# Kernel tuning notes

Measured on AMD Instinct MI355X. Metric: run time of the kernel, lower is better.

The kernel has to match this reference:

```python
import jax, jax.numpy as jnp
import numpy as np
import math

B, T, C, H = 2, 2048, 1024, 16
HD = C // H
WINDOW = 256  # local_attn_ctx with attnblocksize=1


def setup_inputs() -> dict:
    key = jax.random.key(0)
    k1, k2, k3 = jax.random.split(key, 3)
    x = jax.random.normal(k1, (B, T, C), dtype=jnp.float32)
    Wqkv = jax.random.normal(k2, (C, 3 * C), dtype=jnp.float32) * 0.02
    bqkv = jnp.zeros((3 * C,), dtype=jnp.float32)
    Wproj = jax.random.normal(k3, (C, C), dtype=jnp.float32) * 0.02
    bproj = jnp.zeros((C,), dtype=jnp.float32)
    # 'local' block-sparse layout at token granularity: causal + sliding window
    i = np.arange(T)[:, None]
    j = np.arange(T)[None, :]
    mask = ((j <= i) & (i - j <= WINDOW)).astype(np.int32)
    return {"x": x, "Wqkv": Wqkv, "bqkv": bqkv, "Wproj": Wproj, "bproj": bproj,
            "mask": jnp.asarray(mask)}


def reference(x, Wqkv, bqkv, Wproj, bproj, mask):
    Bb, Tt, Cc = x.shape
    qkv = (x @ Wqkv + bqkv).reshape(Bb, Tt, 3, H, HD)  # [B,T,3,H,hd]
    q = jnp.transpose(qkv[:, :, 0], (0, 2, 1, 3))  # [B,H,T,hd]
    k = jnp.transpose(qkv[:, :, 1], (0, 2, 1, 3))
    v = jnp.transpose(qkv[:, :, 2], (0, 2, 1, 3))
    scale = 1.0 / math.sqrt(HD)
    att = jnp.einsum('bhqd,bhkd->bhqk', q, k) * scale  # dense T x T scores
    att = jnp.where(mask[:Tt, :Tt] == 0, -jnp.inf, att)
    att = jax.nn.softmax(att, axis=-1)
    y = jnp.einsum('bhqk,bhkd->bhqd', att, v)
    y = jnp.transpose(y, (0, 2, 1, 3)).reshape(Bb, Tt, Cc)
    return y @ Wproj + bproj
```

## Files before the change

### kernel.cpp

```cpp
#include <hip/hip_runtime.h>
#include <hip/hip_bf16.h>
#include <math.h>

typedef __bf16 bf16;
typedef __attribute__((ext_vector_type(8))) __bf16 bf16x8;
typedef __attribute__((ext_vector_type(4))) __bf16 bf16x4;
typedef __attribute__((ext_vector_type(4))) float f32x4;

#define B_  2
#define T_  2048
#define C_  1024
#define H_  16
#define HD_ 64
#define WIN_ 256

#define GLOAD16(g, l)                                                        \
  __builtin_amdgcn_global_load_lds(                                          \
      (const __attribute__((address_space(1))) void*)(g),                    \
      (__attribute__((address_space(3))) void*)(l), 16, 0, 0)


__global__ __launch_bounds__(256) void cvt_f32_bf16_k(const float* __restrict__ in,
                                                      bf16* __restrict__ out) {
  int idx = blockIdx.x * 256 + threadIdx.x;
  const float4 v = ((const float4*)in)[idx];
  bf16x4 o;
  o[0] = (bf16)v.x; o[1] = (bf16)v.y; o[2] = (bf16)v.z; o[3] = (bf16)v.w;
  ((bf16x4*)out)[idx] = o;
}

__global__ __launch_bounds__(256) void transpose_cvt_k(const float* __restrict__ W,
                                                       bf16* __restrict__ WT,
                                                       int K, int N) {
  __shared__ float t[32][33];
  int n0 = blockIdx.x * 32, k0 = blockIdx.y * 32;
  int tx = threadIdx.x, ty = threadIdx.y;
  #pragma unroll
  for (int i = 0; i < 32; i += 8)
    t[ty + i][tx] = W[(size_t)(k0 + ty + i) * N + (n0 + tx)];
  __syncthreads();
  #pragma unroll
  for (int i = 0; i < 32; i += 8)
    WT[(size_t)(n0 + ty + i) * K + (k0 + tx)] = (bf16)t[tx][ty + i];
}


template <int TM, int TN, int WM, int WN, int MODE>
__global__ __launch_bounds__(WM * WN * 64, 2)
void gemm_dp_k(const bf16* __restrict__ A, const bf16* __restrict__ Bt,
               const float* __restrict__ bias,
               void* __restrict__ out0, void* __restrict__ out1,
               int M, int N, int K) {
  constexpr int NW    = WM * WN;
  constexpr int WROWS = TM / WM;
  constexpr int WCOLS = TN / WN;
  constexpr int FM    = WROWS / 16;
  constexpr int FN    = WCOLS / 16;
  constexpr int CA    = TM / 16 / NW;
  constexpr int CB    = TN / 16 / NW;

  const int bm = blockIdx.x * TM;
  const int bn = blockIdx.y * TN;
  const int tid  = threadIdx.x;
  const int wid  = tid >> 6;
  const int lane = tid & 63;
  const int wr = wid / WN;
  const int wc = wid % WN;
  const int lr = lane & 15;
  const int g  = lane >> 4;

  __shared__ bf16 As[4][TM][32];
  __shared__ bf16 Bs[4][TN][32];

  f32x4 acc[FM][FN] = {};

  const int rloc = lane >> 2;
  const int scol = (((lane & 3) ^ (rloc & 3))) * 8;
  const bf16* aSrc = A  + (size_t)(bm + wid * CA * 16 + rloc) * K + scol;
  const bf16* bSrc = Bt + (size_t)(bn + wid * CB * 16 + rloc) * K + scol;

  #define STAGE_DP(buf, kt)                                                   \
    do {                                                                      \
      _Pragma("unroll")                                                       \
      for (int i = 0; i < CA; ++i)                                            \
        GLOAD16(aSrc + (size_t)(i * 16) * K + (kt) * 32,                      \
                &As[buf][(wid * CA + i) * 16][0]);                            \
      _Pragma("unroll")                                                       \
      for (int i = 0; i < CB; ++i)                                            \
        GLOAD16(bSrc + (size_t)(i * 16) * K + (kt) * 32,                      \
                &Bs[buf][(wid * CB + i) * 16][0]);                            \
    } while (0)

  const int NT = K >> 5;
  const int kc = (g ^ (lr & 3)) * 8;

  STAGE_DP(0, 0);
  STAGE_DP(1, 1);

  for (int t = 0; t < NT; ++t) {
    const int buf = t & 3;
    if (t + 2 < NT) {
      STAGE_DP((t + 2) & 3, t + 2);
      asm volatile("s_waitcnt vmcnt(8)" ::: "memory");
    } else if (t + 1 < NT) {
      asm volatile("s_waitcnt vmcnt(4)" ::: "memory");
    } else {
      asm volatile("s_waitcnt vmcnt(0)" ::: "memory");
    }
    __builtin_amdgcn_s_barrier();
    asm volatile("" ::: "memory");

    bf16x8 af[FM], bfv[FN];
    #pragma unroll
    for (int m = 0; m < FM; ++m)
      af[m] = *(const bf16x8*)&As[buf][wr * WROWS + m * 16 + lr][kc];
    #pragma unroll
    for (int n = 0; n < FN; ++n)
      bfv[n] = *(const bf16x8*)&Bs[buf][wc * WCOLS + n * 16 + lr][kc];

    __builtin_amdgcn_s_setprio(1);
    #pragma unroll
    for (int m = 0; m < FM; ++m)
      #pragma unroll
      for (int n = 0; n < FN; ++n)
        acc[m][n] = __builtin_amdgcn_mfma_f32_16x16x32_bf16(af[m], bfv[n], acc[m][n], 0, 0, 0);
    __builtin_amdgcn_s_setprio(0);
  }
  #undef STAGE_DP

  const int orow = g * 4;
  #pragma unroll
  for (int n = 0; n < FN; ++n) {
    const int nbase = bn + wc * WCOLS + n * 16;
    const int gn = nbase + lr;
    const float bv = bias[gn];
    #pragma unroll
    for (int m = 0; m < FM; ++m) {
      const int gm0 = bm + wr * WROWS + m * 16 + orow;
      if (MODE == 0) {
        #pragma unroll
        for (int r = 0; r < 4; ++r)
          ((float*)out0)[(size_t)(gm0 + r) * N + gn] = acc[m][n][r] + bv;
      } else {
        if (nbase < 2 * C_) {
          #pragma unroll
          for (int r = 0; r < 4; ++r)
            ((bf16*)out0)[(size_t)(gm0 + r) * (2 * C_) + gn] = (bf16)(acc[m][n][r] + bv);
        } else {
          const int vcol = gn - 2 * C_;
          const int h = vcol >> 6, d = vcol & 63;
          const int b = gm0 >> 11, tok = gm0 & (T_ - 1);
          bf16x4 o;
          #pragma unroll
          for (int r = 0; r < 4; ++r) o[r] = (bf16)(acc[m][n][r] + bv);
          *(bf16x4*)&((bf16*)out1)[(((size_t)b * H_ + h) * HD_ + d) * T_ + tok] = o;
        }
      }
    }
  }
}


__global__ __launch_bounds__(256) void attn_mfma_k(const bf16* __restrict__ qk,
                                                   const bf16* __restrict__ vt,
                                                   bf16* __restrict__ y) {
  const int q0 = blockIdx.x * 64;
  const int h  = blockIdx.y;
  const int b  = blockIdx.z;
  const int tid  = threadIdx.x;
  const int wid  = tid >> 6;
  const int lane = tid & 63;
  const int lr = lane & 15;
  const int g  = lane >> 4;

  __shared__ bf16 Ks[64][72];
  __shared__ bf16 Vs[64][72];
  __shared__ bf16 Ps[4][16][72];

  const int qrow = q0 + wid * 16 + lr;
  const bf16* qptr = qk + ((size_t)(b * T_ + qrow)) * (2 * C_) + h * HD_;
  bf16x8 qf[2];
  qf[0] = *(const bf16x8*)(qptr + g * 8);
  qf[1] = *(const bf16x8*)(qptr + 32 + g * 8);

  float m = -1e30f, l = 0.f;
  f32x4 yacc[4] = {};

  const int kt_lo = (blockIdx.x >= 4) ? (int)blockIdx.x - 4 : 0;
  for (int kt = kt_lo; kt <= (int)blockIdx.x; ++kt) {
    __syncthreads();
    #pragma unroll
    for (int i = 0; i < 2; ++i) {
      int cc = tid + i * 256;
      int rr = cc >> 3;
      int c0 = (cc & 7) * 8;
      *(bf16x8*)&Ks[rr][c0] = *(const bf16x8*)&qk[((size_t)(b * T_) + kt * 64 + rr) * (2 * C_) + C_ + h * HD_ + c0];
      *(bf16x8*)&Vs[rr][c0] = *(const bf16x8*)&vt[(((size_t)b * H_ + h) * HD_ + rr) * T_ + kt * 64 + c0];
    }
    __syncthreads();

    f32x4 sacc[4] = {};
    #pragma unroll
    for (int t = 0; t < 4; ++t)
      #pragma unroll
      for (int s = 0; s < 2; ++s)
        sacc[t] = __builtin_amdgcn_mfma_f32_16x16x32_bf16(
            *(const bf16x8*)&Ks[t * 16 + lr][s * 32 + g * 8], qf[s], sacc[t], 0, 0, 0);

    float pv[4][4];
    float rmax = -1e30f;
    #pragma unroll
    for (int t = 0; t < 4; ++t)
      #pragma unroll
      for (int r = 0; r < 4; ++r) {
        const int key = kt * 64 + t * 16 + g * 4 + r;
        const bool valid = (key <= qrow) && (qrow - key <= WIN_);
        const float sv = valid ? sacc[t][r] * 0.125f : -__builtin_inff();
        pv[t][r] = sv;
        rmax = fmaxf(rmax, sv);
      }
    rmax = fmaxf(rmax, __shfl_xor(rmax, 16));
    rmax = fmaxf(rmax, __shfl_xor(rmax, 32));

    const float mnew = fmaxf(m, rmax);
    const float alpha = __expf(m - mnew);
    m = mnew;
    float lsum = 0.f;
    #pragma unroll
    for (int t = 0; t < 4; ++t)
      #pragma unroll
      for (int r = 0; r < 4; ++r) {
        const float e = __expf(pv[t][r] - mnew);
        pv[t][r] = e;
        lsum += e;
      }
    lsum += __shfl_xor(lsum, 16);
    lsum += __shfl_xor(lsum, 32);
    l = l * alpha + lsum;

    #pragma unroll
    for (int t = 0; t < 4; ++t) {
      bf16x4 pk;
      #pragma unroll
      for (int r = 0; r < 4; ++r) pk[r] = (bf16)pv[t][r];
      *(bf16x4*)&Ps[wid][lr][t * 16 + g * 4] = pk;
    }

    float al[4];
    #pragma unroll
    for (int r = 0; r < 4; ++r) al[r] = __shfl(alpha, g * 4 + r);
    #pragma unroll
    for (int t = 0; t < 4; ++t)
      #pragma unroll
      for (int r = 0; r < 4; ++r) yacc[t][r] *= al[r];

    bf16x8 pf[2];
    pf[0] = *(const bf16x8*)&Ps[wid][lr][g * 8];
    pf[1] = *(const bf16x8*)&Ps[wid][lr][32 + g * 8];
    #pragma unroll
    for (int t = 0; t < 4; ++t)
      #pragma unroll
      for (int s = 0; s < 2; ++s)
        yacc[t] = __builtin_amdgcn_mfma_f32_16x16x32_bf16(
            pf[s], *(const bf16x8*)&Vs[t * 16 + lr][s * 32 + g * 8], yacc[t], 0, 0, 0);
  }

  float li[4];
  #pragma unroll
  for (int r = 0; r < 4; ++r) li[r] = 1.f / __shfl(l, g * 4 + r);
  #pragma unroll
  for (int t = 0; t < 4; ++t)
    #pragma unroll
    for (int r = 0; r < 4; ++r) {
      const int tok = q0 + wid * 16 + g * 4 + r;
      y[((size_t)(b * T_ + tok)) * C_ + h * HD_ + t * 16 + lr] = (bf16)(yacc[t][r] * li[r]);
    }
}


extern "C" void kernel_launch(void* const* d_in, const int* in_sizes, int n_in,
                              void* d_out, int out_size, void* d_ws, size_t ws_size,
                              hipStream_t stream) {
  const float* x     = (const float*)d_in[0];
  const float* Wqkv  = (const float*)d_in[1];
  const float* bqkv  = (const float*)d_in[2];
  const float* Wproj = (const float*)d_in[3];
  const float* bproj = (const float*)d_in[4];
  float* out = (float*)d_out;

  const size_t SZ_QK  = (size_t)B_ * T_ * 2 * C_ * sizeof(bf16);
  const size_t SZ_VT  = (size_t)B_ * H_ * HD_ * T_ * sizeof(bf16);
  const size_t SZ_XB  = (size_t)B_ * T_ * C_ * sizeof(bf16);
  const size_t SZ_WQT = (size_t)3 * C_ * C_ * sizeof(bf16);
  const size_t SZ_WPT = (size_t)C_ * C_ * sizeof(bf16);
  const size_t NEED   = SZ_QK + SZ_VT + SZ_XB + SZ_WQT + SZ_WPT + SZ_XB;
  if (ws_size < NEED) return;

  char* ws = (char*)d_ws;
  bf16* qkb    = (bf16*)(ws);
  bf16* vtb    = (bf16*)(ws + SZ_QK);
  bf16* xb     = (bf16*)(ws + SZ_QK + SZ_VT);
  bf16* wqkvT  = (bf16*)(ws + SZ_QK + SZ_VT + SZ_XB);
  bf16* wprojT = (bf16*)(ws + SZ_QK + SZ_VT + SZ_XB + SZ_WQT);
  bf16* yb     = (bf16*)(ws + SZ_QK + SZ_VT + SZ_XB + SZ_WQT + SZ_WPT);

  cvt_f32_bf16_k<<<4096, 256, 0, stream>>>(x, xb);
  transpose_cvt_k<<<dim3(3 * C_ / 32, C_ / 32), dim3(32, 8), 0, stream>>>(Wqkv, wqkvT, C_, 3 * C_);
  transpose_cvt_k<<<dim3(C_ / 32, C_ / 32), dim3(32, 8), 0, stream>>>(Wproj, wprojT, C_, C_);

  gemm_dp_k<256, 256, 2, 4, 2><<<dim3((B_ * T_) / 256, (3 * C_) / 256), 512, 0, stream>>>(
      xb, wqkvT, bqkv, qkb, vtb, B_ * T_, 3 * C_, C_);

  attn_mfma_k<<<dim3(T_ / 64, H_, B_), 256, 0, stream>>>(qkb, vtb, yb);

  gemm_dp_k<128, 128, 2, 2, 0><<<dim3((B_ * T_) / 128, C_ / 128), 256, 0, stream>>>(
      yb, wprojT, bproj, out, nullptr, B_ * T_, C_, C_);
}
```

Baseline: 96.77 us.

## Add 8-phase pipelined QKV GEMM with XOR-swizzled LDS and split prefetch

```diff
diff --git a/kernel.cpp b/kernel.cpp
--- a/kernel.cpp
+++ b/kernel.cpp
@@ -18,6 +18,12 @@
   __builtin_amdgcn_global_load_lds(                                          \
       (const __attribute__((address_space(1))) void*)(g),                    \
       (__attribute__((address_space(3))) void*)(l), 16, 0, 0)
+
+__device__ inline void bar() {
+  asm volatile("" ::: "memory");
+  __builtin_amdgcn_s_barrier();
+  asm volatile("" ::: "memory");
+}
 
 
 __global__ __launch_bounds__(256) void cvt_f32_bf16_k(const float* __restrict__ in,
@@ -42,6 +48,152 @@
   #pragma unroll
   for (int i = 0; i < 32; i += 8)
     WT[(size_t)(n0 + ty + i) * K + (k0 + tx)] = (bf16)t[tx][ty + i];
+}
+
+
+template <int MODE>
+__global__ __launch_bounds__(512, 2) void gemm8p_k(const bf16* __restrict__ A,
+                                                   const bf16* __restrict__ Bt,
+                                                   const float* __restrict__ bias,
+                                                   void* __restrict__ out0,
+                                                   void* __restrict__ out1,
+                                                   int M, int N, int K) {
+  const int bm = blockIdx.x * 256;
+  const int bn = blockIdx.y * 256;
+  const int tid  = threadIdx.x;
+  const int wid  = tid >> 6;
+  const int lane = tid & 63;
+  const int wr = wid >> 2;
+  const int wc = wid & 3;
+  const int lr = lane & 15;
+  const int g  = lane >> 4;
+
+  __shared__ bf16 As[2][256 * 64];
+  __shared__ bf16 Bs[2][256 * 64];
+
+  f32x4 acc[8][4] = {};
+
+  const int sr = lane >> 3;
+  const int sc = ((lane & 7) ^ sr) << 3;
+  const bf16* aS = A  + (size_t)(bm + wid * 8 + sr) * K + sc;
+  const bf16* bS = Bt + (size_t)(bn + wid * 8 + sr) * K + sc;
+
+  #define STA(p_, q_, u_)                                                    \
+    GLOAD16(aS + (size_t)((q_) * 64) * K + (u_) * 64,                        \
+            &As[p_][((q_) * 64 + wid * 8) * 64])
+  #define STB(p_, q_, u_)                                                    \
+    GLOAD16(bS + (size_t)((q_) * 64) * K + (u_) * 64,                        \
+            &Bs[p_][((q_) * 64 + wid * 8) * 64])
+
+  const int NT  = K >> 6;
+  const int kc0 = ((g    ) ^ (lr & 7)) << 3;
+  const int kc1 = ((4 + g) ^ (lr & 7)) << 3;
+
+  STA(0, 0, 0); STA(0, 2, 0); STA(0, 1, 0); STA(0, 3, 0);
+  STB(0, 0, 0); STB(0, 1, 0); STB(0, 2, 0); STB(0, 3, 0);
+  STA(1, 0, 1); STA(1, 2, 1);
+  asm volatile("s_waitcnt vmcnt(2)" ::: "memory");
+  __builtin_amdgcn_s_barrier();
+  asm volatile("" ::: "memory");
+
+  #define MFMA16(mb, a0_, a1_, a2_, a3_)                                     \
+    do {                                                                     \
+      __builtin_amdgcn_s_setprio(1);                                         \
+      _Pragma("unroll")                                                      \
+      for (int n = 0; n < 4; ++n) {                                          \
+        acc[(mb) + 0][n] = __builtin_amdgcn_mfma_f32_16x16x32_bf16(a0_, bv[n], acc[(mb) + 0][n], 0, 0, 0); \
+        acc[(mb) + 1][n] = __builtin_amdgcn_mfma_f32_16x16x32_bf16(a1_, bv[n], acc[(mb) + 1][n], 0, 0, 0); \
+        acc[(mb) + 2][n] = __builtin_amdgcn_mfma_f32_16x16x32_bf16(a2_, bv[n], acc[(mb) + 2][n], 0, 0, 0); \
+        acc[(mb) + 3][n] = __builtin_amdgcn_mfma_f32_16x16x32_bf16(a3_, bv[n], acc[(mb) + 3][n], 0, 0, 0); \
+      }                                                                      \
+      __builtin_amdgcn_s_setprio(0);                                         \
+    } while (0)
+
+  for (int u = 0; u < NT; ++u) {
+    const int p  = u & 1;
+    const int pn = p ^ 1;
+    const bf16* Ar = &As[p][(wr * 128 + lr) * 64];
+    const bf16* Br = &Bs[p][(wc * 64  + lr) * 64];
+    bf16x8 bv[4], a0, a1, a2, a3;
+
+    #pragma unroll
+    for (int n = 0; n < 4; ++n) bv[n] = *(const bf16x8*)(Br + n * 1024 + kc0);
+    a0 = *(const bf16x8*)(Ar + 0 * 1024 + kc0);
+    a1 = *(const bf16x8*)(Ar + 1 * 1024 + kc0);
+    a2 = *(const bf16x8*)(Ar + 2 * 1024 + kc0);
+    a3 = *(const bf16x8*)(Ar + 3 * 1024 + kc0);
+    if (u + 1 < NT) { STA(pn, 1, u + 1); STA(pn, 3, u + 1); }
+    bar();
+    MFMA16(0, a0, a1, a2, a3);
+    if (u + 1 < NT) asm volatile("s_waitcnt vmcnt(8)" ::: "memory");
+    else            asm volatile("s_waitcnt vmcnt(0)" ::: "memory");
+    bar();
+
+    a0 = *(const bf16x8*)(Ar + 4 * 1024 + kc0);
+    a1 = *(const bf16x8*)(Ar + 5 * 1024 + kc0);
+    a2 = *(const bf16x8*)(Ar + 6 * 1024 + kc0);
+    a3 = *(const bf16x8*)(Ar + 7 * 1024 + kc0);
+    if (u + 1 < NT) { STB(pn, 0, u + 1); STB(pn, 1, u + 1); }
+    bar();
+    MFMA16(4, a0, a1, a2, a3);
+    bar();
+
+    #pragma unroll
+    for (int n = 0; n < 4; ++n) bv[n] = *(const bf16x8*)(Br + n * 1024 + kc1);
+    a0 = *(const bf16x8*)(Ar + 0 * 1024 + kc1);
+    a1 = *(const bf16x8*)(Ar + 1 * 1024 + kc1);
+    a2 = *(const bf16x8*)(Ar + 2 * 1024 + kc1);
+    a3 = *(const bf16x8*)(Ar + 3 * 1024 + kc1);
+    if (u + 1 < NT) { STB(pn, 2, u + 1); STB(pn, 3, u + 1); }
+    bar();
+    MFMA16(0, a0, a1, a2, a3);
+    bar();
+
+    a0 = *(const bf16x8*)(Ar + 4 * 1024 + kc1);
+    a1 = *(const bf16x8*)(Ar + 5 * 1024 + kc1);
+    a2 = *(const bf16x8*)(Ar + 6 * 1024 + kc1);
+    a3 = *(const bf16x8*)(Ar + 7 * 1024 + kc1);
+    if (u + 2 < NT) { STA(p, 0, u + 2); STA(p, 2, u + 2); }
+    bar();
+    MFMA16(4, a0, a1, a2, a3);
+    if (u + 2 < NT) asm volatile("s_waitcnt vmcnt(2)" ::: "memory");
+    else            asm volatile("s_waitcnt vmcnt(0)" ::: "memory");
+    bar();
+  }
+  #undef MFMA16
+  #undef STA
+  #undef STB
+
+  const int orow = g * 4;
+  #pragma unroll
+  for (int n = 0; n < 4; ++n) {
+    const int nbase = bn + wc * 64 + n * 16;
+    const int gn = nbase + lr;
+    const float bv_ = bias[gn];
+    #pragma unroll
+    for (int m = 0; m < 8; ++m) {
+      const int gm0 = bm + wr * 128 + m * 16 + orow;
+      if (MODE == 0) {
+        #pragma unroll
+        for (int r = 0; r < 4; ++r)
+          ((float*)out0)[(size_t)(gm0 + r) * N + gn] = acc[m][n][r] + bv_;
+      } else {
+        if (nbase < 2 * C_) {
+          #pragma unroll
+          for (int r = 0; r < 4; ++r)
+            ((bf16*)out0)[(size_t)(gm0 + r) * (2 * C_) + gn] = (bf16)(acc[m][n][r] + bv_);
+        } else {
+          const int vcol = gn - 2 * C_;
+          const int h = vcol >> 6, d = vcol & 63;
+          const int b = gm0 >> 11, tok = gm0 & (T_ - 1);
+          bf16x4 o;
+          #pragma unroll
+          for (int r = 0; r < 4; ++r) o[r] = (bf16)(acc[m][n][r] + bv_);
+          *(bf16x4*)&((bf16*)out1)[(((size_t)b * H_ + h) * HD_ + d) * T_ + tok] = o;
+        }
+      }
+    }
+  }
 }
 
 
@@ -131,8 +283,7 @@
   const int orow = g * 4;
   #pragma unroll
   for (int n = 0; n < FN; ++n) {
-    const int nbase = bn + wc * WCOLS + n * 16;
-    const int gn = nbase + lr;
+    const int gn = bn + wc * WCOLS + n * 16 + lr;
     const float bv = bias[gn];
     #pragma unroll
     for (int m = 0; m < FM; ++m) {
@@ -141,20 +292,6 @@
         #pragma unroll
         for (int r = 0; r < 4; ++r)
           ((float*)out0)[(size_t)(gm0 + r) * N + gn] = acc[m][n][r] + bv;
-      } else {
-        if (nbase < 2 * C_) {
-          #pragma unroll
-          for (int r = 0; r < 4; ++r)
-            ((bf16*)out0)[(size_t)(gm0 + r) * (2 * C_) + gn] = (bf16)(acc[m][n][r] + bv);
-        } else {
-          const int vcol = gn - 2 * C_;
-          const int h = vcol >> 6, d = vcol & 63;
-          const int b = gm0 >> 11, tok = gm0 & (T_ - 1);
-          bf16x4 o;
-          #pragma unroll
-          for (int r = 0; r < 4; ++r) o[r] = (bf16)(acc[m][n][r] + bv);
-          *(bf16x4*)&((bf16*)out1)[(((size_t)b * H_ + h) * HD_ + d) * T_ + tok] = o;
-        }
       }
     }
   }
@@ -308,7 +445,7 @@
   transpose_cvt_k<<<dim3(3 * C_ / 32, C_ / 32), dim3(32, 8), 0, stream>>>(Wqkv, wqkvT, C_, 3 * C_);
   transpose_cvt_k<<<dim3(C_ / 32, C_ / 32), dim3(32, 8), 0, stream>>>(Wproj, wprojT, C_, C_);
 
-  gemm_dp_k<256, 256, 2, 4, 2><<<dim3((B_ * T_) / 256, (3 * C_) / 256), 512, 0, stream>>>(
+  gemm8p_k<2><<<dim3((B_ * T_) / 256, (3 * C_) / 256), 512, 0, stream>>>(
       xb, wqkvT, bqkv, qkb, vtb, B_ * T_, 3 * C_, C_);
 
   attn_mfma_k<<<dim3(T_ / 64, H_, B_), 256, 0, stream>>>(qkb, vtb, yb);
```

Result: no change. 97.06 us (+0.3%).

## Restructure GEMM staging to double-buffered BK=64 with smaller tiles

Applied to the files above, without the earlier changes.

```diff
diff --git a/kernel.cpp b/kernel.cpp
--- a/kernel.cpp
+++ b/kernel.cpp
@@ -18,6 +18,12 @@
   __builtin_amdgcn_global_load_lds(                                          \
       (const __attribute__((address_space(1))) void*)(g),                    \
       (__attribute__((address_space(3))) void*)(l), 16, 0, 0)
+
+__device__ inline void bar() {
+  asm volatile("" ::: "memory");
+  __builtin_amdgcn_s_barrier();
+  asm volatile("" ::: "memory");
+}
 
 
 __global__ __launch_bounds__(256) void cvt_f32_bf16_k(const float* __restrict__ in,
@@ -45,9 +51,9 @@
 }
 
 
-template <int TM, int TN, int WM, int WN, int MODE>
-__global__ __launch_bounds__(WM * WN * 64, 2)
-void gemm_dp_k(const bf16* __restrict__ A, const bf16* __restrict__ Bt,
+template <int TM, int TN, int WM, int WN, int MINW, int MODE>
+__global__ __launch_bounds__(WM * WN * 64, MINW)
+void gemm_db_k(const bf16* __restrict__ A, const bf16* __restrict__ Bt,
                const float* __restrict__ bias,
                void* __restrict__ out0, void* __restrict__ out1,
                int M, int N, int K) {
@@ -56,8 +62,8 @@
   constexpr int WCOLS = TN / WN;
   constexpr int FM    = WROWS / 16;
   constexpr int FN    = WCOLS / 16;
-  constexpr int CA    = TM / 16 / NW;
-  constexpr int CB    = TN / 16 / NW;
+  constexpr int NCH   = (TM + TN) / 8;
+  constexpr int CPW   = NCH / NW;
 
   const int bm = blockIdx.x * TM;
   const int bn = blockIdx.y * TN;
@@ -69,90 +75,97 @@
   const int lr = lane & 15;
   const int g  = lane >> 4;
 
-  __shared__ bf16 As[4][TM][32];
-  __shared__ bf16 Bs[4][TN][32];
+  __shared__ bf16 As[2][TM * 64];
+  __shared__ bf16 Bs[2][TN * 64];
 
   f32x4 acc[FM][FN] = {};
 
-  const int rloc = lane >> 2;
-  const int scol = (((lane & 3) ^ (rloc & 3))) * 8;
-  const bf16* aSrc = A  + (size_t)(bm + wid * CA * 16 + rloc) * K + scol;
-  const bf16* bSrc = Bt + (size_t)(bn + wid * CB * 16 + rloc) * K + scol;
-
-  #define STAGE_DP(buf, kt)                                                   \
-    do {                                                                      \
-      _Pragma("unroll")                                                       \
-      for (int i = 0; i < CA; ++i)                                            \
-        GLOAD16(aSrc + (size_t)(i * 16) * K + (kt) * 32,                      \
-                &As[buf][(wid * CA + i) * 16][0]);                            \
-      _Pragma("unroll")                                                       \
-      for (int i = 0; i < CB; ++i)                                            \
-        GLOAD16(bSrc + (size_t)(i * 16) * K + (kt) * 32,                      \
-                &Bs[buf][(wid * CB + i) * 16][0]);                            \
+  const int sr = lane >> 3;
+  const int sc = ((lane & 7) ^ sr) << 3;
+
+  #define STG(p_, u_)                                                        \
+    do {                                                                     \
+      _Pragma("unroll")                                                      \
+      for (int i = 0; i < CPW; ++i) {                                        \
+        const int c = wid * CPW + i;                                         \
+        if (c < TM / 8) {                                                    \
+          GLOAD16(A + (size_t)(bm + c * 8 + sr) * K + (u_) * 64 + sc,        \
+                  &As[p_][c * 8 * 64]);                                      \
+        } else {                                                             \
+          GLOAD16(Bt + (size_t)(bn + (c - TM / 8) * 8 + sr) * K + (u_) * 64 + sc, \
+                  &Bs[p_][(c - TM / 8) * 8 * 64]);                           \
+        }                                                                    \
+      }                                                                      \
     } while (0)
 
-  const int NT = K >> 5;
-  const int kc = (g ^ (lr & 3)) * 8;
-
-  STAGE_DP(0, 0);
-  STAGE_DP(1, 1);
-
-  for (int t = 0; t < NT; ++t) {
-    const int buf = t & 3;
-    if (t + 2 < NT) {
-      STAGE_DP((t + 2) & 3, t + 2);
-      asm volatile("s_waitcnt vmcnt(8)" ::: "memory");
-    } else if (t + 1 < NT) {
-      asm volatile("s_waitcnt vmcnt(4)" ::: "memory");
+  const int NT = K >> 6;
+  const int kc0 = ((0 + g) ^ (lr & 7)) << 3;
+  const int kc1 = ((4 + g) ^ (lr & 7)) << 3;
+
+  STG(0, 0);
+  asm volatile("s_waitcnt vmcnt(0)" ::: "memory");
+  __builtin_amdgcn_s_barrier();
+  asm volatile("" ::: "memory");
+
+  for (int u = 0; u < NT; ++u) {
+    const int p = u & 1;
+    if (u + 1 < NT) {
+      STG(p ^ 1, u + 1);
+      asm volatile("s_waitcnt vmcnt(%0)" :: "i"(CPW) : "memory");
     } else {
       asm volatile("s_waitcnt vmcnt(0)" ::: "memory");
     }
-    __builtin_amdgcn_s_barrier();
-    asm volatile("" ::: "memory");
-
-    bf16x8 af[FM], bfv[FN];
-    #pragma unroll
-    for (int m = 0; m < FM; ++m)
-      af[m] = *(const bf16x8*)&As[buf][wr * WROWS + m * 16 + lr][kc];
-    #pragma unroll
-    for (int n = 0; n < FN; ++n)
-      bfv[n] = *(const bf16x8*)&Bs[buf][wc * WCOLS + n * 16 + lr][kc];
-
-    __builtin_amdgcn_s_setprio(1);
-    #pragma unroll
-    for (int m = 0; m < FM; ++m)
+    bar();
+
+    const bf16* Ar = &As[p][(wr * WROWS + lr) * 64];
+    const bf16* Br = &Bs[p][(wc * WCOLS + lr) * 64];
+    #pragma unroll
+    for (int s = 0; s < 2; ++s) {
+      const int kc = s ? kc1 : kc0;
+      bf16x8 av[FM], bvv[FN];
+      #pragma unroll
+      for (int m = 0; m < FM; ++m)
+        av[m] = *(const bf16x8*)(Ar + m * 16 * 64 + kc);
       #pragma unroll
       for (int n = 0; n < FN; ++n)
-        acc[m][n] = __builtin_amdgcn_mfma_f32_16x16x32_bf16(af[m], bfv[n], acc[m][n], 0, 0, 0);
-    __builtin_amdgcn_s_setprio(0);
+        bvv[n] = *(const bf16x8*)(Br + n * 16 * 64 + kc);
+      __builtin_amdgcn_s_setprio(1);
+      #pragma unroll
+      for (int m = 0; m < FM; ++m)
+        #pragma unroll
+        for (int n = 0; n < FN; ++n)
+          acc[m][n] = __builtin_amdgcn_mfma_f32_16x16x32_bf16(av[m], bvv[n], acc[m][n], 0, 0, 0);
+      __builtin_amdgcn_s_setprio(0);
+    }
+    bar();
   }
-  #undef STAGE_DP
+  #undef STG
 
   const int orow = g * 4;
   #pragma unroll
   for (int n = 0; n < FN; ++n) {
     const int nbase = bn + wc * WCOLS + n * 16;
     const int gn = nbase + lr;
-    const float bv = bias[gn];
+    const float bv_ = bias[gn];
     #pragma unroll
     for (int m = 0; m < FM; ++m) {
       const int gm0 = bm + wr * WROWS + m * 16 + orow;
       if (MODE == 0) {
         #pragma unroll
         for (int r = 0; r < 4; ++r)
-          ((float*)out0)[(size_t)(gm0 + r) * N + gn] = acc[m][n][r] + bv;
+          ((float*)out0)[(size_t)(gm0 + r) * N + gn] = acc[m][n][r] + bv_;
       } else {
         if (nbase < 2 * C_) {
           #pragma unroll
           for (int r = 0; r < 4; ++r)
-            ((bf16*)out0)[(size_t)(gm0 + r) * (2 * C_) + gn] = (bf16)(acc[m][n][r] + bv);
+            ((bf16*)out0)[(size_t)(gm0 + r) * (2 * C_) + gn] = (bf16)(acc[m][n][r] + bv_);
         } else {
           const int vcol = gn - 2 * C_;
           const int h = vcol >> 6, d = vcol & 63;
           const int b = gm0 >> 11, tok = gm0 & (T_ - 1);
           bf16x4 o;
           #pragma unroll
-          for (int r = 0; r < 4; ++r) o[r] = (bf16)(acc[m][n][r] + bv);
+          for (int r = 0; r < 4; ++r) o[r] = (bf16)(acc[m][n][r] + bv_);
           *(bf16x4*)&((bf16*)out1)[(((size_t)b * H_ + h) * HD_ + d) * T_ + tok] = o;
         }
       }
@@ -308,11 +321,11 @@
   transpose_cvt_k<<<dim3(3 * C_ / 32, C_ / 32), dim3(32, 8), 0, stream>>>(Wqkv, wqkvT, C_, 3 * C_);
   transpose_cvt_k<<<dim3(C_ / 32, C_ / 32), dim3(32, 8), 0, stream>>>(Wproj, wprojT, C_, C_);
 
-  gemm_dp_k<256, 256, 2, 4, 2><<<dim3((B_ * T_) / 256, (3 * C_) / 256), 512, 0, stream>>>(
+  gemm_db_k<128, 192, 2, 4, 4, 2><<<dim3((B_ * T_) / 128, (3 * C_) / 192), 512, 0, stream>>>(
       xb, wqkvT, bqkv, qkb, vtb, B_ * T_, 3 * C_, C_);
 
   attn_mfma_k<<<dim3(T_ / 64, H_, B_), 256, 0, stream>>>(qkb, vtb, yb);
 
-  gemm_dp_k<128, 128, 2, 2, 0><<<dim3((B_ * T_) / 128, C_ / 128), 256, 0, stream>>>(
+  gemm_db_k<64, 128, 2, 2, 2, 0><<<dim3((B_ * T_) / 64, C_ / 128), 256, 0, stream>>>(
       yb, wprojT, bproj, out, nullptr, B_ * T_, C_, C_);
 }
```

Measured after the change: 84.92 us. -12.2%, faster.
